# Kernel tuning notes

Hardware: AMD Instinct MI355X
Metric: run time of the kernel (lower is better)

## Reference

```python
import math
import jax, jax.numpy as jnp
import numpy as np

SAMPLE_RATE = 44100.0
R_PARAM = 0.5   # resonance buffer 'r'
F_PARAM = 1000.0  # cutoff buffer 'f'


def setup_inputs() -> dict:
    key = jax.random.key(0)
    k1, k2, k3 = jax.random.split(key, 3)
    B = 4194304
    u_n = jax.random.normal(k1, (B, 1, 1), dtype=jnp.float32)
    x_n1 = jax.random.normal(k2, (B, 4, 1), dtype=jnp.float32)
    u_n1 = jax.random.normal(k3, (B, 1, 1), dtype=jnp.float32)
    # learned scalar parameters (initial values from the module)
    gf = jnp.float32(1.6071)
    gr = jnp.float32(0.9993)
    gain = jnp.float32(3.9415)
    alpha = jnp.float32(0.8782)
    return {"u_n": u_n, "x_n1": x_n1, "u_n1": u_n1,
            "gf": gf, "gr": gr, "gain": gain, "alpha": alpha,
            "batch_size": B}


def _build_mats(gf, gr, gain, alpha):
    k = jnp.float32(1.0 / SAMPLE_RATE)
    w = 2.0 * math.pi * gf * F_PARAM  # 2*pi*gf*f
    z = jnp.zeros_like(w)
    A = jnp.stack([
        jnp.stack([-w, z, z, -4.0 * w * gr * R_PARAM]),
        jnp.stack([w, -w, z, z]),
        jnp.stack([z, w, -w, z]),
        jnp.stack([z, z, w, -w]),
    ])  # [4,4]
    Bv = jnp.stack([w, z, z, z])[:, None]  # [4,1]
    C = jnp.stack([z, z, z, gain])[None, :]  # [1,4]
    I = jnp.eye(4, dtype=jnp.float32)
    kA2 = k * A / 2.0
    M_inv = jnp.linalg.inv(I - kA2 * alpha)          # inv(I - k*A/2*alpha)
    M_fwd = I + 2.0 * kA2 - kA2 * alpha              # I + k*A - k*A/2*alpha
    kb2 = k * Bv / 2.0
    b_a = kb2 * alpha                                # [4,1]
    b_1ma = kb2 * (1.0 - alpha / 2.0)                # [4,1]
    return M_inv, M_fwd, b_a, b_1ma, C


def reference(u_n, x_n1, u_n1, gf, gr, gain, alpha, batch_size):
    M_inv, M_fwd, b_a, b_1ma, C = _build_mats(gf, gr, gain, alpha)
    # rhs: [B,4,1] = M_fwd @ x_n1 + b_a*u_n + b_1ma*u_n1 (u terms are scalar per sample)
    rhs = jnp.einsum('ij,bjo->bio', M_fwd, x_n1) + b_a[None] * u_n + b_1ma[None] * u_n1
    x_n = jnp.einsum('ij,bjo->bio', M_inv, rhs)      # [B,4,1]
    y_n = jnp.einsum('ij,bjo->bio', C, x_n)          # [B,1,1]
    return (y_n, x_n, u_n)
```

## Files before the change

### kernel.cpp

```cpp
#include <hip/hip_runtime.h>
#include <math.h>

#define SAMPLE_RATE 44100.0
#define R_PARAM 0.5
#define F_PARAM 1000.0

__device__ void inv4x4(const double A[4][4], double Ainv[4][4]) {
    double M[4][8];
    for (int i = 0; i < 4; ++i) {
        for (int j = 0; j < 4; ++j) { M[i][j] = A[i][j]; M[i][4 + j] = (i == j) ? 1.0 : 0.0; }
    }
    for (int col = 0; col < 4; ++col) {
        int p = col;
        for (int r = col + 1; r < 4; ++r)
            if (fabs(M[r][col]) > fabs(M[p][col])) p = r;
        if (p != col)
            for (int j = 0; j < 8; ++j) { double t = M[col][j]; M[col][j] = M[p][j]; M[p][j] = t; }
        double d = 1.0 / M[col][col];
        for (int j = 0; j < 8; ++j) M[col][j] *= d;
        for (int r = 0; r < 4; ++r) {
            if (r == col) continue;
            double f = M[r][col];
            for (int j = 0; j < 8; ++j) M[r][j] -= f * M[col][j];
        }
    }
    for (int i = 0; i < 4; ++i)
        for (int j = 0; j < 4; ++j) Ainv[i][j] = M[i][4 + j];
}

__global__ void moog_prologue(const float* __restrict__ gf,
                              const float* __restrict__ gr,
                              const float* __restrict__ gain,
                              const float* __restrict__ alpha,
                              float* __restrict__ ws) {
    const double k  = 1.0 / SAMPLE_RATE;
    const double w  = 2.0 * M_PI * (double)gf[0] * F_PARAM;
    const double grv = (double)gr[0];
    const double al  = (double)alpha[0];
    const double gn  = (double)gain[0];

    double A[4][4] = {
        { -w, 0.0, 0.0, -4.0 * w * grv * R_PARAM },
        {  w,  -w, 0.0, 0.0 },
        { 0.0,  w,  -w, 0.0 },
        { 0.0, 0.0,  w,  -w }
    };

    double kA2[4][4];
    for (int i = 0; i < 4; ++i)
        for (int j = 0; j < 4; ++j) kA2[i][j] = 0.5 * k * A[i][j];

    double Mlhs[4][4];
    for (int i = 0; i < 4; ++i)
        for (int j = 0; j < 4; ++j)
            Mlhs[i][j] = ((i == j) ? 1.0 : 0.0) - kA2[i][j] * al;

    double Minv[4][4];
    inv4x4(Mlhs, Minv);

    double Mfwd[4][4];
    for (int i = 0; i < 4; ++i)
        for (int j = 0; j < 4; ++j)
            Mfwd[i][j] = ((i == j) ? 1.0 : 0.0) + kA2[i][j] * (2.0 - al);

    double Mc[4][4];
    for (int i = 0; i < 4; ++i)
        for (int j = 0; j < 4; ++j) {
            double s = 0.0;
            for (int m = 0; m < 4; ++m) s += Minv[i][m] * Mfwd[m][j];
            Mc[i][j] = s;
        }

    double kb2_0 = 0.5 * k * w;
    double ba0  = kb2_0 * al;
    double b1m0 = kb2_0 * (1.0 - 0.5 * al);

    for (int i = 0; i < 4; ++i) {
        for (int j = 0; j < 4; ++j) ws[4 * i + j] = (float)Mc[i][j];
        ws[16 + i] = (float)(Minv[i][0] * ba0);
        ws[20 + i] = (float)(Minv[i][0] * b1m0);
    }
    ws[24] = (float)gn;
}

__global__ __launch_bounds__(256) void moog_main(
        const float*  __restrict__ u_n,
        const float4* __restrict__ x_n1,
        const float*  __restrict__ u_n1,
        const float*  __restrict__ ws,
        float* __restrict__ out,
        int B) {
    __shared__ float c[25];
    int t = threadIdx.x;
    if (t < 25) c[t] = ws[t];
    __syncthreads();

    int i = blockIdx.x * blockDim.x + t;
    if (i >= B) return;

    float4 x = x_n1[i];
    float u  = u_n[i];
    float u1 = u_n1[i];

    float r0 = c[0]  * x.x + c[1]  * x.y + c[2]  * x.z + c[3]  * x.w + c[16] * u + c[20] * u1;
    float r1 = c[4]  * x.x + c[5]  * x.y + c[6]  * x.z + c[7]  * x.w + c[17] * u + c[21] * u1;
    float r2 = c[8]  * x.x + c[9]  * x.y + c[10] * x.z + c[11] * x.w + c[18] * u + c[22] * u1;
    float r3 = c[12] * x.x + c[13] * x.y + c[14] * x.z + c[15] * x.w + c[19] * u + c[23] * u1;

    out[i] = c[24] * r3;
    float4* ox = (float4*)(out + B);
    ox[i] = make_float4(r0, r1, r2, r3);
    out[5 * (size_t)B + i] = u;
}

extern "C" void kernel_launch(void* const* d_in, const int* in_sizes, int n_in,
                              void* d_out, int out_size, void* d_ws, size_t ws_size,
                              hipStream_t stream) {
    const float* u_n   = (const float*)d_in[0];
    const float* x_n1  = (const float*)d_in[1];
    const float* u_n1  = (const float*)d_in[2];
    const float* gf    = (const float*)d_in[3];
    const float* gr    = (const float*)d_in[4];
    const float* gain  = (const float*)d_in[5];
    const float* alpha = (const float*)d_in[6];

    int B = in_sizes[0];
    float* ws = (float*)d_ws;

    moog_prologue<<<1, 1, 0, stream>>>(gf, gr, gain, alpha, ws);

    int block = 256;
    int grid = (B + block - 1) / block;
    moog_main<<<grid, block, 0, stream>>>(u_n, (const float4*)x_n1, u_n1, ws,
                                          (float*)d_out, B);
}
```

Before: 192.5 us.

## Process four samples per thread with vectorized scalar I/O and nontemporal stores

Adds a kernel in which each thread loads u and u1 as float4 vectors, stages them in shared memory, and computes four samples per thread. The y outputs go through shared memory so they can be written as vectorized stores. All outputs use nontemporal stores. The aim is to cut the number of scalar memory transactions on this bandwidth-bound kernel, at the cost of extra shared memory and two block barriers. The old kernel stays as a fallback for B not divisible by four, and its x output is now written as scalar stores.

New measurement: 195.4 us. Within noise of the previous version (+1.5%).

```diff
diff --git a/kernel.cpp b/kernel.cpp
--- a/kernel.cpp
+++ b/kernel.cpp
@@ -4,6 +4,8 @@
 #define SAMPLE_RATE 44100.0
 #define R_PARAM 0.5
 #define F_PARAM 1000.0
+
+typedef float f32x4 __attribute__((ext_vector_type(4)));
 
 __device__ void inv4x4(const double A[4][4], double Ainv[4][4]) {
     double M[4][8];
@@ -83,6 +85,66 @@
     ws[24] = (float)gn;
 }
 
+__global__ __launch_bounds__(256) void moog_main_v3(
+        const f32x4* __restrict__ u4,
+        const f32x4* __restrict__ x4,
+        const f32x4* __restrict__ u14,
+        const float* __restrict__ ws,
+        float* __restrict__ out,
+        int B) {
+    __shared__ float c[25];
+    __shared__ float su[1024];
+    __shared__ float su1[1024];
+    __shared__ float sy[1024];
+
+    int t = threadIdx.x;
+    if (t < 25) c[t] = ws[t];
+
+    int nq = B >> 2;
+    int qb = blockIdx.x << 8;
+    int q  = qb + t;
+    bool valid = q < nq;
+
+    f32x4* ou = (f32x4*)(out + 5 * (size_t)B);
+    if (valid) {
+        f32x4 u  = u4[q];
+        f32x4 u1 = u14[q];
+        *(f32x4*)&su[4 * t]  = u;
+        *(f32x4*)&su1[4 * t] = u1;
+        __builtin_nontemporal_store(u, &ou[q]);
+    }
+    __syncthreads();
+
+    int sbase = qb << 2;
+    f32x4* ox = (f32x4*)(out + (size_t)B);
+
+    #pragma unroll
+    for (int k = 0; k < 4; ++k) {
+        int idx = (k << 8) + t;
+        int s = sbase + idx;
+        if (s < B) {
+            f32x4 x = x4[s];
+            float u  = su[idx];
+            float u1 = su1[idx];
+
+            float r0 = c[0]  * x.x + c[1]  * x.y + c[2]  * x.z + c[3]  * x.w + c[16] * u + c[20] * u1;
+            float r1 = c[4]  * x.x + c[5]  * x.y + c[6]  * x.z + c[7]  * x.w + c[17] * u + c[21] * u1;
+            float r2 = c[8]  * x.x + c[9]  * x.y + c[10] * x.z + c[11] * x.w + c[18] * u + c[22] * u1;
+            float r3 = c[12] * x.x + c[13] * x.y + c[14] * x.z + c[15] * x.w + c[19] * u + c[23] * u1;
+
+            f32x4 xv = {r0, r1, r2, r3};
+            __builtin_nontemporal_store(xv, &ox[s]);
+            sy[idx] = c[24] * r3;
+        }
+    }
+    __syncthreads();
+
+    if (valid) {
+        f32x4 yq = *(f32x4*)&sy[4 * t];
+        __builtin_nontemporal_store(yq, &((f32x4*)out)[q]);
+    }
+}
+
 __global__ __launch_bounds__(256) void moog_main(
         const float*  __restrict__ u_n,
         const float4* __restrict__ x_n1,
@@ -108,8 +170,8 @@
     float r3 = c[12] * x.x + c[13] * x.y + c[14] * x.z + c[15] * x.w + c[19] * u + c[23] * u1;
 
     out[i] = c[24] * r3;
-    float4* ox = (float4*)(out + B);
-    ox[i] = make_float4(r0, r1, r2, r3);
+    float* ox = out + (size_t)B + 4 * (size_t)i;
+    ox[0] = r0; ox[1] = r1; ox[2] = r2; ox[3] = r3;
     out[5 * (size_t)B + i] = u;
 }
 
@@ -130,7 +192,15 @@
     moog_prologue<<<1, 1, 0, stream>>>(gf, gr, gain, alpha, ws);
 
     int block = 256;
-    int grid = (B + block - 1) / block;
-    moog_main<<<grid, block, 0, stream>>>(u_n, (const float4*)x_n1, u_n1, ws,
-                                          (float*)d_out, B);
-}
+    if ((B & 3) == 0) {
+        int nq = B >> 2;
+        int grid = (nq + block - 1) / block;
+        moog_main_v3<<<grid, block, 0, stream>>>((const f32x4*)u_n, (const f32x4*)x_n1,
+                                                 (const f32x4*)u_n1, ws,
+                                                 (float*)d_out, B);
+    } else {
+        int grid = (B + block - 1) / block;
+        moog_main<<<grid, block, 0, stream>>>(u_n, (const float4*)x_n1, u_n1, ws,
+                                              (float*)d_out, B);
+    }
+}
```

## Use persistent fixed-grid kernel processing four elements per thread per iteration

Applied to the files above, without the earlier changes.

Adds a kernel launched with a fixed grid of 512 blocks, each looping over a contiguous chunk of samples and handling four samples per thread per iteration, with loads batched ahead of compute to raise memory-level parallelism. The fallback kernel now writes the state output as scalar stores rather than a float4 store, dropping the 16-byte alignment assumption. The aim is to cut launch and scheduling overhead and keep more loads in flight on a bandwidth-bound kernel. The fixed grid may underfill the GPU or give uneven tails.

New measurement: 203.1 us. +5.5%, slower.

```diff
diff --git a/kernel.cpp b/kernel.cpp
--- a/kernel.cpp
+++ b/kernel.cpp
@@ -4,6 +4,8 @@
 #define SAMPLE_RATE 44100.0
 #define R_PARAM 0.5
 #define F_PARAM 1000.0
+
+typedef float f32x4 __attribute__((ext_vector_type(4)));
 
 __device__ void inv4x4(const double A[4][4], double Ainv[4][4]) {
     double M[4][8];
@@ -83,6 +85,81 @@
     ws[24] = (float)gn;
 }
 
+__global__ __launch_bounds__(256) void moog_main_v4(
+        const float* __restrict__ u_n,
+        const f32x4* __restrict__ x4,
+        const float* __restrict__ u_n1,
+        const float* __restrict__ ws,
+        float* __restrict__ out,
+        int B, int S) {
+    __shared__ float c[25];
+    int t = threadIdx.x;
+    if (t < 25) c[t] = ws[t];
+    __syncthreads();
+
+    float* oy = out;
+    f32x4* ox = (f32x4*)(out + (size_t)B);
+    float* ou = out + 5 * (size_t)B;
+
+    size_t base = (size_t)blockIdx.x * (size_t)S;
+    size_t end  = base + (size_t)S;
+    if (base >= (size_t)B) return;
+    if (end > (size_t)B) end = (size_t)B;
+
+    for (size_t j0 = base; j0 < end; j0 += 1024) {
+        size_t s0 = j0 + (size_t)t;
+
+        float u[4];
+        f32x4 x[4];
+        float u1[4];
+        bool  v[4];
+
+        #pragma unroll
+        for (int k = 0; k < 4; ++k) {
+            size_t s = s0 + (size_t)(k << 8);
+            v[k] = s < (size_t)B;
+            if (v[k]) u[k] = u_n[s];
+        }
+        #pragma unroll
+        for (int k = 0; k < 4; ++k) {
+            size_t s = s0 + (size_t)(k << 8);
+            if (v[k]) x[k] = x4[s];
+        }
+        #pragma unroll
+        for (int k = 0; k < 4; ++k) {
+            size_t s = s0 + (size_t)(k << 8);
+            if (v[k]) u1[k] = u_n1[s];
+        }
+
+        float r0[4], r1[4], r2[4], r3[4];
+        #pragma unroll
+        for (int k = 0; k < 4; ++k) {
+            if (v[k]) {
+                r0[k] = c[0]  * x[k].x + c[1]  * x[k].y + c[2]  * x[k].z + c[3]  * x[k].w + c[16] * u[k] + c[20] * u1[k];
+                r1[k] = c[4]  * x[k].x + c[5]  * x[k].y + c[6]  * x[k].z + c[7]  * x[k].w + c[17] * u[k] + c[21] * u1[k];
+                r2[k] = c[8]  * x[k].x + c[9]  * x[k].y + c[10] * x[k].z + c[11] * x[k].w + c[18] * u[k] + c[22] * u1[k];
+                r3[k] = c[12] * x[k].x + c[13] * x[k].y + c[14] * x[k].z + c[15] * x[k].w + c[19] * u[k] + c[23] * u1[k];
+            }
+        }
+
+        #pragma unroll
+        for (int k = 0; k < 4; ++k) {
+            size_t s = s0 + (size_t)(k << 8);
+            if (v[k]) oy[s] = c[24] * r3[k];
+        }
+        #pragma unroll
+        for (int k = 0; k < 4; ++k) {
+            size_t s = s0 + (size_t)(k << 8);
+            if (v[k]) { f32x4 xv = {r0[k], r1[k], r2[k], r3[k]}; ox[s] = xv; }
+        }
+        #pragma unroll
+        for (int k = 0; k < 4; ++k) {
+            size_t s = s0 + (size_t)(k << 8);
+            if (v[k]) ou[s] = u[k];
+        }
+    }
+}
+
 __global__ __launch_bounds__(256) void moog_main(
         const float*  __restrict__ u_n,
         const float4* __restrict__ x_n1,
@@ -108,8 +185,8 @@
     float r3 = c[12] * x.x + c[13] * x.y + c[14] * x.z + c[15] * x.w + c[19] * u + c[23] * u1;
 
     out[i] = c[24] * r3;
-    float4* ox = (float4*)(out + B);
-    ox[i] = make_float4(r0, r1, r2, r3);
+    float* ox = out + (size_t)B + 4 * (size_t)i;
+    ox[0] = r0; ox[1] = r1; ox[2] = r2; ox[3] = r3;
     out[5 * (size_t)B + i] = u;
 }
 
@@ -129,8 +206,16 @@
 
     moog_prologue<<<1, 1, 0, stream>>>(gf, gr, gain, alpha, ws);
 
-    int block = 256;
-    int grid = (B + block - 1) / block;
-    moog_main<<<grid, block, 0, stream>>>(u_n, (const float4*)x_n1, u_n1, ws,
-                                          (float*)d_out, B);
-}
+    if ((B & 3) == 0) {
+        const int grid = 512;
+        long long per = ((long long)B + (long long)grid * 1024 - 1) / ((long long)grid * 1024);
+        int S = (int)(per * 1024);
+        moog_main_v4<<<grid, 256, 0, stream>>>(u_n, (const f32x4*)x_n1, u_n1, ws,
+                                               (float*)d_out, B, S);
+    } else {
+        int block = 256;
+        int grid = (B + block - 1) / block;
+        moog_main<<<grid, block, 0, stream>>>(u_n, (const float4*)x_n1, u_n1, ws,
+                                              (float*)d_out, B);
+    }
+}
```
